# Optimization experiments

Hardware: AMD Instinct MI355X
Metric: run time of the kernel (lower is better)

The kernel has to match this reference:

```python
import jax, jax.numpy as jnp
import numpy as np

D_MODEL = 1024
NUM_SYMBOLS = 1024
NUM_VALUES = 1024
GRAPH_STEPS = 3
BATCH = 64


def setup_inputs() -> dict:
    key = jax.random.key(0)
    ks = jax.random.split(key, 12)
    B, S, V, D = BATCH, NUM_SYMBOLS, NUM_VALUES, D_MODEL
    scale = 0.02
    return {
        "map_memory": jax.random.normal(ks[0], (B, S, V), jnp.float32) * scale,
        "step_memory": jax.random.normal(ks[1], (B, S, S), jnp.float32) * scale,
        "query_idx": jax.random.randint(ks[2], (B,), 0, S),
        "query_mask": jnp.ones((B,), jnp.float32),
        "symbol_bank": jax.random.normal(ks[3], (S, D), jnp.float32) * scale,
        "value_bank": jax.random.normal(ks[4], (V, D), jnp.float32) * scale,
        "Wo1": jax.random.normal(ks[5], (D, D), jnp.float32) * scale,
        "bo1": jnp.zeros((D,), jnp.float32),
        "Wo2": jax.random.normal(ks[6], (D, V), jnp.float32) * scale,
        "bo2": jnp.zeros((V,), jnp.float32),
        "Wf1": jax.random.normal(ks[7], (D, D), jnp.float32) * scale,
        "bf1": jnp.zeros((D,), jnp.float32),
        "Wf2": jax.random.normal(ks[8], (D, D), jnp.float32) * scale,
        "bf2": jnp.zeros((D,), jnp.float32),
    }


def reference(map_memory, step_memory, query_idx, query_mask,
              symbol_bank, value_bank,
              Wo1, bo1, Wo2, bo2, Wf1, bf1, Wf2, bf2):
    # query_state: [B, S] one-hot masked
    query_state = jax.nn.one_hot(query_idx, NUM_SYMBOLS, dtype=jnp.float32)
    query_state = query_state * query_mask[:, None]

    acc_values = jnp.einsum('bs,bsv->bv', query_state, map_memory)   # [B, V]
    acc_symbols = jnp.einsum('bs,sd->bd', query_state, symbol_bank)  # [B, D]

    def walk_step(carry, _):
        walk, values, symbols = carry
        next_walk = jnp.einsum('bs,bst->bt', walk, step_memory)
        next_values = values + jnp.einsum('bs,bsv->bv', next_walk, map_memory)
        next_symbols = symbols + jnp.einsum('bs,sd->bd', next_walk, symbol_bank)
        return (next_walk, next_values, next_symbols), None

    (_, acc_values, acc_symbols), _ = jax.lax.scan(
        walk_step, (query_state, acc_values, acc_symbols), xs=None,
        length=GRAPH_STEPS)

    graph_state = acc_symbols + jnp.einsum('bv,vd->bd', acc_values, value_bank)

    logits = jax.nn.gelu(graph_state @ Wo1 + bo1) @ Wo2 + bo2      # [B, V]
    feedback = jax.nn.gelu(graph_state @ Wf1 + bf1) @ Wf2 + bf2    # [B, D]
    return logits, feedback
```

## Files before the change

kernel.cpp:

```cpp
#include <hip/hip_runtime.h>

#define BB 64
#define SS 1024
#define NN 1024

template<int KC, int GATHER, int REV>
__global__ __launch_bounds__(256) void k_walk(const float* __restrict__ A,
                                              const float* __restrict__ W,
                                              float* __restrict__ C,
                                              const int* __restrict__ qidx,
                                              const float* __restrict__ qmask) {
    const int k0 = blockIdx.x * KC;
    const int b  = REV ? (gridDim.y - 1 - blockIdx.y) : blockIdx.y;

    __shared__ float As[KC];
    if (threadIdx.x < KC) {
        float v;
        if (GATHER) {
            int q = qidx[b];
            v = qmask[b] * W[(size_t)b * SS * SS + (size_t)q * SS + k0 + threadIdx.x];
        } else {
            v = A[b * NN + k0 + threadIdx.x];
        }
        As[threadIdx.x] = v;
    }
    __syncthreads();

    const float* Wp = W + (size_t)b * SS * SS + (size_t)k0 * NN + threadIdx.x * 4;
    float acc0 = 0.f, acc1 = 0.f, acc2 = 0.f, acc3 = 0.f;
    for (int k = 0; k < KC; ++k) {
        float4 wv = *(const float4*)(Wp + (size_t)k * NN);
        float a = As[k];
        acc0 = fmaf(a, wv.x, acc0);
        acc1 = fmaf(a, wv.y, acc1);
        acc2 = fmaf(a, wv.z, acc2);
        acc3 = fmaf(a, wv.w, acc3);
    }
    float* c = C + (size_t)b * NN + threadIdx.x * 4;
    unsafeAtomicAdd(c + 0, acc0);
    unsafeAtomicAdd(c + 1, acc1);
    unsafeAtomicAdd(c + 2, acc2);
    unsafeAtomicAdd(c + 3, acc3);
}

template<int ROWS, int KC>
__global__ __launch_bounds__(256) void k_small(const float* __restrict__ A0,
                                               const float* __restrict__ W0,
                                               float* __restrict__ C0,
                                               const float* __restrict__ A1,
                                               const float* __restrict__ W1,
                                               float* __restrict__ C1) {
    const float* A = blockIdx.z ? A1 : A0;
    const float* W = blockIdx.z ? W1 : W0;
    float*       C = blockIdx.z ? C1 : C0;
    const int k0 = blockIdx.x * KC;
    const int r0 = blockIdx.y * ROWS;

    __shared__ float As[ROWS * KC];
    for (int i = threadIdx.x; i < ROWS * KC; i += 256) {
        int r = i / KC, k = i % KC;
        As[i] = A[(r0 + r) * NN + k0 + k];
    }
    __syncthreads();

    const float* Wp = W + (size_t)k0 * NN + threadIdx.x * 4;
    float acc[ROWS][4];
    #pragma unroll
    for (int r = 0; r < ROWS; ++r) {
        acc[r][0] = 0.f; acc[r][1] = 0.f; acc[r][2] = 0.f; acc[r][3] = 0.f;
    }
    for (int k = 0; k < KC; ++k) {
        float4 wv = *(const float4*)(Wp + (size_t)k * NN);
        #pragma unroll
        for (int r = 0; r < ROWS; ++r) {
            float a = As[r * KC + k];
            acc[r][0] = fmaf(a, wv.x, acc[r][0]);
            acc[r][1] = fmaf(a, wv.y, acc[r][1]);
            acc[r][2] = fmaf(a, wv.z, acc[r][2]);
            acc[r][3] = fmaf(a, wv.w, acc[r][3]);
        }
    }
    const int t = threadIdx.x * 4;
    #pragma unroll
    for (int r = 0; r < ROWS; ++r) {
        float* c = C + (size_t)(r0 + r) * NN + t;
        unsafeAtomicAdd(c + 0, acc[r][0]);
        unsafeAtomicAdd(c + 1, acc[r][1]);
        unsafeAtomicAdd(c + 2, acc[r][2]);
        unsafeAtomicAdd(c + 3, acc[r][3]);
    }
}

__global__ void k_wsum(const float* __restrict__ SM,
                       const float* __restrict__ w2, const float* __restrict__ w3,
                       const int* __restrict__ qidx, const float* __restrict__ qmask,
                       float* __restrict__ Wsum) {
    int b = blockIdx.x;
    int q = qidx[b];
    float m = qmask[b];
    const float* row = SM + (size_t)b * SS * SS + (size_t)q * SS;
    int t = threadIdx.x * 4;
    #pragma unroll
    for (int j = 0; j < 4; ++j) {
        int s = t + j;
        float v = m * row[s] + w2[b * SS + s] + w3[b * SS + s];
        if (s == q) v += m;
        Wsum[b * SS + s] = v;
    }
}

__global__ void k_biasgelu(float* __restrict__ h0, float* __restrict__ h1,
                           const float* __restrict__ b0, const float* __restrict__ b1) {
    float* h = blockIdx.y ? h1 : h0;
    const float* bias = blockIdx.y ? b1 : b0;
    int b = blockIdx.x;
    int t = threadIdx.x * 4;
    #pragma unroll
    for (int j = 0; j < 4; ++j) {
        int d = t + j;
        float x = h[b * NN + d] + bias[d];
        float c = 0.7978845608028654f * (x + 0.044715f * x * x * x);
        h[b * NN + d] = 0.5f * x * (1.0f + tanhf(c));
    }
}

__global__ void k_out(const float* __restrict__ lg, const float* __restrict__ fb,
                      const float* __restrict__ bo2, const float* __restrict__ bf2,
                      float* __restrict__ out) {
    int half = blockIdx.y;
    const float* src = half ? fb : lg;
    const float* bias = half ? bf2 : bo2;
    float* dst = out + (size_t)half * BB * NN;
    int b = blockIdx.x;
    int t = threadIdx.x * 4;
    #pragma unroll
    for (int j = 0; j < 4; ++j) {
        int n = t + j;
        dst[b * NN + n] = src[b * NN + n] + bias[n];
    }
}

extern "C" void kernel_launch(void* const* d_in, const int* in_sizes, int n_in,
                              void* d_out, int out_size, void* d_ws, size_t ws_size,
                              hipStream_t stream) {
    const float* MM   = (const float*)d_in[0];
    const float* SM   = (const float*)d_in[1];
    const int*   qidx = (const int*)d_in[2];
    const float* qmask= (const float*)d_in[3];
    const float* sb   = (const float*)d_in[4];
    const float* vb   = (const float*)d_in[5];
    const float* Wo1  = (const float*)d_in[6];
    const float* bo1  = (const float*)d_in[7];
    const float* Wo2  = (const float*)d_in[8];
    const float* bo2  = (const float*)d_in[9];
    const float* Wf1  = (const float*)d_in[10];
    const float* bf1  = (const float*)d_in[11];
    const float* Wf2  = (const float*)d_in[12];
    const float* bf2  = (const float*)d_in[13];
    float* out = (float*)d_out;

    float* ws    = (float*)d_ws;
    float* walk2 = ws;
    float* walk3 = ws + 65536;
    float* accv  = ws + 131072;
    float* gs    = ws + 196608;
    float* h_o   = ws + 262144;
    float* h_f   = ws + 327680;
    float* lg    = ws + 393216;
    float* fb    = ws + 458752;
    float* Wsum  = ws + 524288;

    hipMemsetAsync(d_ws, 0, 524288 * sizeof(float), stream);

    k_walk<64, 1, 0><<<dim3(16, BB), 256, 0, stream>>>(nullptr, SM, walk2, qidx, qmask);
    k_walk<64, 0, 1><<<dim3(16, BB), 256, 0, stream>>>(walk2, SM, walk3, qidx, qmask);
    k_wsum<<<BB, 256, 0, stream>>>(SM, walk2, walk3, qidx, qmask, Wsum);
    k_walk<64, 0, 0><<<dim3(16, BB), 256, 0, stream>>>(Wsum, MM, accv, qidx, qmask);
    k_small<8, 128><<<dim3(8, 8, 2), 256, 0, stream>>>(Wsum, sb, gs, accv, vb, gs);
    k_small<8, 128><<<dim3(8, 8, 2), 256, 0, stream>>>(gs, Wo1, h_o, gs, Wf1, h_f);
    k_biasgelu<<<dim3(BB, 2), 256, 0, stream>>>(h_o, h_f, bo1, bf1);
    k_small<8, 128><<<dim3(8, 8, 2), 256, 0, stream>>>(h_o, Wo2, lg, h_f, Wf2, fb);
    k_out<<<dim3(BB, 2), 256, 0, stream>>>(lg, fb, bo2, bf2, out);
}
```

Before: 765.0 us.

## Replace walk atomics with partial-sum buffers and stream map memory nontemporally

Walk kernels now write per-K-chunk partial results to separate buffers, and the next consumer reduces them, instead of accumulating with global float atomics. The map_memory pass uses nontemporal loads to avoid polluting cache with the large one-shot stream. This removes the atomic traffic and most of the workspace memset, at the cost of extra partial-buffer reads and a larger workspace.

```diff
diff --git a/kernel.cpp b/kernel.cpp
--- a/kernel.cpp
+++ b/kernel.cpp
@@ -3,63 +3,102 @@
 #define BB 64
 #define SS 1024
 #define NN 1024
-
-template<int KC, int GATHER, int REV>
-__global__ __launch_bounds__(256) void k_walk(const float* __restrict__ A,
-                                              const float* __restrict__ W,
-                                              float* __restrict__ C,
-                                              const int* __restrict__ qidx,
-                                              const float* __restrict__ qmask) {
-    const int k0 = blockIdx.x * KC;
-    const int b  = REV ? (gridDim.y - 1 - blockIdx.y) : blockIdx.y;
+#define PARTS 16
+#define KC 64
+
+typedef float f4 __attribute__((ext_vector_type(4)));
+
+template<int ASRC, int REV, int NT>
+__global__ __launch_bounds__(256) void k_walkp(const float* __restrict__ A,
+                                               const float* __restrict__ P,
+                                               const float* __restrict__ W,
+                                               float* __restrict__ Cp,
+                                               const int* __restrict__ qidx,
+                                               const float* __restrict__ qmask) {
+    const int part = blockIdx.x;
+    const int b    = REV ? (gridDim.y - 1 - blockIdx.y) : blockIdx.y;
+    const int k0   = part * KC;
 
     __shared__ float As[KC];
     if (threadIdx.x < KC) {
         float v;
-        if (GATHER) {
+        if (ASRC == 0) {
             int q = qidx[b];
             v = qmask[b] * W[(size_t)b * SS * SS + (size_t)q * SS + k0 + threadIdx.x];
+        } else if (ASRC == 1) {
+            v = 0.f;
+            #pragma unroll
+            for (int p = 0; p < PARTS; ++p)
+                v += P[(size_t)p * BB * SS + b * SS + k0 + threadIdx.x];
         } else {
-            v = A[b * NN + k0 + threadIdx.x];
+            v = A[b * SS + k0 + threadIdx.x];
         }
         As[threadIdx.x] = v;
     }
     __syncthreads();
 
     const float* Wp = W + (size_t)b * SS * SS + (size_t)k0 * NN + threadIdx.x * 4;
-    float acc0 = 0.f, acc1 = 0.f, acc2 = 0.f, acc3 = 0.f;
+    f4 acc = {0.f, 0.f, 0.f, 0.f};
     for (int k = 0; k < KC; ++k) {
-        float4 wv = *(const float4*)(Wp + (size_t)k * NN);
+        f4 wv;
+        if (NT) wv = __builtin_nontemporal_load((const f4*)(Wp + (size_t)k * NN));
+        else    wv = *(const f4*)(Wp + (size_t)k * NN);
         float a = As[k];
-        acc0 = fmaf(a, wv.x, acc0);
-        acc1 = fmaf(a, wv.y, acc1);
-        acc2 = fmaf(a, wv.z, acc2);
-        acc3 = fmaf(a, wv.w, acc3);
-    }
-    float* c = C + (size_t)b * NN + threadIdx.x * 4;
-    unsafeAtomicAdd(c + 0, acc0);
-    unsafeAtomicAdd(c + 1, acc1);
-    unsafeAtomicAdd(c + 2, acc2);
-    unsafeAtomicAdd(c + 3, acc3);
-}
-
-template<int ROWS, int KC>
+        acc.x = fmaf(a, wv.x, acc.x);
+        acc.y = fmaf(a, wv.y, acc.y);
+        acc.z = fmaf(a, wv.z, acc.z);
+        acc.w = fmaf(a, wv.w, acc.w);
+    }
+    f4* c = (f4*)(Cp + (size_t)part * BB * SS + (size_t)b * SS) + threadIdx.x;
+    *c = acc;
+}
+
+__global__ void k_wsum(const float* __restrict__ SM,
+                       const float* __restrict__ P,
+                       const int* __restrict__ qidx, const float* __restrict__ qmask,
+                       float* __restrict__ Wsum) {
+    int b = blockIdx.x;
+    int q = qidx[b];
+    float m = qmask[b];
+    int s0 = threadIdx.x * 4;
+
+    f4 acc = m * (*(const f4*)(SM + (size_t)b * SS * SS + (size_t)q * SS + s0));
+    #pragma unroll
+    for (int p = 0; p < 2 * PARTS; ++p)
+        acc += *(const f4*)(P + (size_t)p * BB * SS + b * SS + s0);
+    int d = q - s0;
+    if (d >= 0 && d < 4) acc[d] += m;
+    *(f4*)(Wsum + b * SS + s0) = acc;
+}
+
+template<int ROWS, int KCS, int AR0, int AR1>
 __global__ __launch_bounds__(256) void k_small(const float* __restrict__ A0,
                                                const float* __restrict__ W0,
                                                float* __restrict__ C0,
                                                const float* __restrict__ A1,
                                                const float* __restrict__ W1,
-                                               float* __restrict__ C1) {
+                                               float* __restrict__ C1,
+                                               const float* __restrict__ P) {
+    const int   ar = blockIdx.z ? AR1 : AR0;
     const float* A = blockIdx.z ? A1 : A0;
     const float* W = blockIdx.z ? W1 : W0;
     float*       C = blockIdx.z ? C1 : C0;
-    const int k0 = blockIdx.x * KC;
+    const int k0 = blockIdx.x * KCS;
     const int r0 = blockIdx.y * ROWS;
 
-    __shared__ float As[ROWS * KC];
-    for (int i = threadIdx.x; i < ROWS * KC; i += 256) {
-        int r = i / KC, k = i % KC;
-        As[i] = A[(r0 + r) * NN + k0 + k];
+    __shared__ float As[ROWS * KCS];
+    for (int i = threadIdx.x; i < ROWS * KCS; i += 256) {
+        int r = i / KCS, k = i % KCS;
+        float v;
+        if (ar) {
+            v = 0.f;
+            #pragma unroll
+            for (int p = 0; p < PARTS; ++p)
+                v += P[(size_t)p * BB * SS + (size_t)(r0 + r) * SS + k0 + k];
+        } else {
+            v = A[(r0 + r) * NN + k0 + k];
+        }
+        As[i] = v;
     }
     __syncthreads();
 
@@ -69,11 +108,11 @@
     for (int r = 0; r < ROWS; ++r) {
         acc[r][0] = 0.f; acc[r][1] = 0.f; acc[r][2] = 0.f; acc[r][3] = 0.f;
     }
-    for (int k = 0; k < KC; ++k) {
+    for (int k = 0; k < KCS; ++k) {
         float4 wv = *(const float4*)(Wp + (size_t)k * NN);
         #pragma unroll
         for (int r = 0; r < ROWS; ++r) {
-            float a = As[r * KC + k];
+            float a = As[r * KCS + k];
             acc[r][0] = fmaf(a, wv.x, acc[r][0]);
             acc[r][1] = fmaf(a, wv.y, acc[r][1]);
             acc[r][2] = fmaf(a, wv.z, acc[r][2]);
@@ -88,24 +127,6 @@
         unsafeAtomicAdd(c + 1, acc[r][1]);
         unsafeAtomicAdd(c + 2, acc[r][2]);
         unsafeAtomicAdd(c + 3, acc[r][3]);
-    }
-}
-
-__global__ void k_wsum(const float* __restrict__ SM,
-                       const float* __restrict__ w2, const float* __restrict__ w3,
-                       const int* __restrict__ qidx, const float* __restrict__ qmask,
-                       float* __restrict__ Wsum) {
-    int b = blockIdx.x;
-    int q = qidx[b];
-    float m = qmask[b];
-    const float* row = SM + (size_t)b * SS * SS + (size_t)q * SS;
-    int t = threadIdx.x * 4;
-    #pragma unroll
-    for (int j = 0; j < 4; ++j) {
-        int s = t + j;
-        float v = m * row[s] + w2[b * SS + s] + w3[b * SS + s];
-        if (s == q) v += m;
-        Wsum[b * SS + s] = v;
     }
 }
 
@@ -159,26 +180,26 @@
     const float* bf2  = (const float*)d_in[13];
     float* out = (float*)d_out;
 
-    float* ws    = (float*)d_ws;
-    float* walk2 = ws;
-    float* walk3 = ws + 65536;
-    float* accv  = ws + 131072;
-    float* gs    = ws + 196608;
-    float* h_o   = ws + 262144;
-    float* h_f   = ws + 327680;
-    float* lg    = ws + 393216;
-    float* fb    = ws + 458752;
-    float* Wsum  = ws + 524288;
-
-    hipMemsetAsync(d_ws, 0, 524288 * sizeof(float), stream);
-
-    k_walk<64, 1, 0><<<dim3(16, BB), 256, 0, stream>>>(nullptr, SM, walk2, qidx, qmask);
-    k_walk<64, 0, 1><<<dim3(16, BB), 256, 0, stream>>>(walk2, SM, walk3, qidx, qmask);
-    k_wsum<<<BB, 256, 0, stream>>>(SM, walk2, walk3, qidx, qmask, Wsum);
-    k_walk<64, 0, 0><<<dim3(16, BB), 256, 0, stream>>>(Wsum, MM, accv, qidx, qmask);
-    k_small<8, 128><<<dim3(8, 8, 2), 256, 0, stream>>>(Wsum, sb, gs, accv, vb, gs);
-    k_small<8, 128><<<dim3(8, 8, 2), 256, 0, stream>>>(gs, Wo1, h_o, gs, Wf1, h_f);
+    float* ws = (float*)d_ws;
+    float* pA   = ws;
+    float* pB   = ws + 1048576;
+    float* pC   = ws + 2097152;
+    float* Wsum = ws + 3145728;
+    float* gs   = ws + 3211264;
+    float* h_o  = ws + 3276800;
+    float* h_f  = ws + 3342336;
+    float* lg   = ws + 3407872;
+    float* fb   = ws + 3473408;
+
+    hipMemsetAsync(gs, 0, 5 * 65536 * sizeof(float), stream);
+
+    k_walkp<0, 0, 0><<<dim3(PARTS, BB), 256, 0, stream>>>(nullptr, nullptr, SM, pA, qidx, qmask);
+    k_walkp<1, 1, 0><<<dim3(PARTS, BB), 256, 0, stream>>>(nullptr, pA, SM, pB, qidx, qmask);
+    k_wsum<<<BB, 256, 0, stream>>>(SM, pA, qidx, qmask, Wsum);
+    k_walkp<2, 0, 1><<<dim3(PARTS, BB), 256, 0, stream>>>(Wsum, nullptr, MM, pC, qidx, qmask);
+    k_small<8, 128, 0, 1><<<dim3(8, 8, 2), 256, 0, stream>>>(Wsum, sb, gs, nullptr, vb, gs, pC);
+    k_small<8, 128, 0, 0><<<dim3(8, 8, 2), 256, 0, stream>>>(gs, Wo1, h_o, gs, Wf1, h_f, nullptr);
     k_biasgelu<<<dim3(BB, 2), 256, 0, stream>>>(h_o, h_f, bo1, bf1);
-    k_small<8, 128><<<dim3(8, 8, 2), 256, 0, stream>>>(h_o, Wo2, lg, h_f, Wf2, fb);
+    k_small<8, 128, 0, 0><<<dim3(8, 8, 2), 256, 0, stream>>>(h_o, Wo2, lg, h_f, Wf2, fb, nullptr);
     k_out<<<dim3(BB, 2), 256, 0, stream>>>(lg, fb, bo2, bf2, out);
 }
```

Result: no change. 754.5 us (-1.4%).
